# Performance work log

Measured on AMD Instinct MI355X. Metric: run time of the kernel, lower is better.

Reference implementation:

```python
import jax, jax.numpy as jnp
import numpy as np

N_NODES = 50000
N_EDGES = 800000
N_FEAT = 128
N_HID = 256
N_PAIRS = 100000


def _gcn_norm(edge_index, n_nodes):
    # add self loops, compute D^-1/2 (A+I) D^-1/2 edge weights (PyG gcn_norm)
    loops = jnp.arange(n_nodes, dtype=edge_index.dtype)
    row = jnp.concatenate([edge_index[0], loops])
    col = jnp.concatenate([edge_index[1], loops])
    deg = jax.ops.segment_sum(jnp.ones_like(col, dtype=jnp.float32), col,
                              num_segments=n_nodes)
    dinv = jnp.where(deg > 0, jax.lax.rsqrt(deg), 0.0)
    norm = dinv[row] * dinv[col]  # [E + N]
    return row, col, norm


def _gcn_conv(x, W, b, row, col, norm, n_nodes):
    h = x @ W                       # [N, out]
    msg = h[row] * norm[:, None]    # gather + scale  [E+N, out]
    agg = jax.ops.segment_sum(msg, col, num_segments=n_nodes)  # scatter-add
    return agg + b


def setup_inputs() -> dict:
    key = jax.random.key(0)
    ks = jax.random.split(key, 9)
    edge_index = jax.random.randint(ks[0], (2, N_EDGES), 0, N_NODES, dtype=jnp.int64)
    features = jax.random.normal(ks[1], (N_NODES, N_FEAT), dtype=jnp.float32)
    mask = jax.random.randint(ks[2], (N_PAIRS, 2), 0, N_NODES, dtype=jnp.int64)
    s1 = 1.0 / np.sqrt(N_FEAT)
    s2 = 1.0 / np.sqrt(N_HID)
    W1 = jax.random.uniform(ks[3], (N_FEAT, N_HID), jnp.float32, -s1, s1)
    b1 = jnp.zeros((N_HID,), jnp.float32)
    W2 = jax.random.uniform(ks[4], (N_HID, N_FEAT), jnp.float32, -s2, s2)
    b2 = jnp.zeros((N_FEAT,), jnp.float32)
    Wl = jax.random.uniform(ks[5], (N_HID, 1), jnp.float32, -s2, s2)
    bl = jax.random.uniform(ks[6], (1,), jnp.float32, -s2, s2)
    return {"edge_index": edge_index, "features": features, "mask": mask,
            "W1": W1, "b1": b1, "W2": W2, "b2": b2, "Wl": Wl, "bl": bl}


def reference(edge_index, features, mask, W1, b1, W2, b2, Wl, bl):
    n = features.shape[0]
    row, col, norm = _gcn_norm(edge_index, n)
    h = _gcn_conv(features, W1, b1, row, col, norm, n)   # GCNConv a
    h = jax.nn.relu(h)                                   # dropout p=0 -> identity
    h = _gcn_conv(h, W2, b2, row, col, norm, n)          # GCNConv b
    mt = mask.T
    p1 = jax.lax.stop_gradient(h[mt[0]])                 # .detach()
    p2 = jax.lax.stop_gradient(h[mt[1]])
    hp = jnp.concatenate([p1, p2], axis=1)               # [n_pairs, 2*n_feat]
    return jax.nn.sigmoid(hp @ Wl + bl)
```

## Files before the change

kernel.cpp:

```cpp
#include <hip/hip_runtime.h>
#include <math.h>

#define NFEAT 128
#define NHID 256
#define NBLK 128

typedef __attribute__((ext_vector_type(8))) short short8;
typedef __attribute__((ext_vector_type(4))) float f32x4;

__device__ inline unsigned short f2bf(float f) {
  unsigned u = __float_as_uint(f);
  u += 0x7fffu + ((u >> 16) & 1u);
  return (unsigned short)(u >> 16);
}
__device__ inline float bflo(unsigned u) { return __uint_as_float(u << 16); }
__device__ inline float bfhi(unsigned u) { return __uint_as_float(u & 0xffff0000u); }


__global__ __launch_bounds__(1024) void k_hist2(const int* __restrict__ col,
                                                int* __restrict__ hist2d,
                                                int nE, int nb) {
  __shared__ int h[1024];
  for (int i = threadIdx.x; i < nb; i += 1024) h[i] = 0;
  __syncthreads();
  int chunk = (nE + NBLK - 1) / NBLK;
  int beg = blockIdx.x * chunk, end = min(beg + chunk, nE);
  for (int e = beg + threadIdx.x; e < end; e += 1024)
    atomicAdd(&h[col[e] >> 6], 1);
  __syncthreads();
  for (int i = threadIdx.x; i < nb; i += 1024)
    hist2d[i * NBLK + blockIdx.x] = h[i];
}

__global__ __launch_bounds__(256) void k_bsum(const int* __restrict__ a,
                                              int* __restrict__ psum, int S) {
  int i = blockIdx.x * 256 + threadIdx.x;
  int v = (i < S) ? a[i] : 0;
#pragma unroll
  for (int o = 32; o; o >>= 1) v += __shfl_down(v, o);
  __shared__ int ws[4];
  if ((threadIdx.x & 63) == 0) ws[threadIdx.x >> 6] = v;
  __syncthreads();
  if (threadIdx.x == 0) psum[blockIdx.x] = ws[0] + ws[1] + ws[2] + ws[3];
}

__global__ __launch_bounds__(1024) void k_s2(const int* __restrict__ psum,
                                             int* __restrict__ pbase, int nc) {
  __shared__ int sh[1024];
  int t = threadIdx.x;
  int v = (t < nc) ? psum[t] : 0;
  sh[t] = v;
  __syncthreads();
  for (int o = 1; o < 1024; o <<= 1) {
    int u = (t >= o) ? sh[t - o] : 0;
    __syncthreads();
    sh[t] += u;
    __syncthreads();
  }
  if (t < nc) pbase[t] = sh[t] - v;
}

__global__ __launch_bounds__(256) void k_s3(const int* __restrict__ a,
                                            const int* __restrict__ pbase,
                                            int* __restrict__ out, int S) {
  __shared__ int sh[256];
  int t = threadIdx.x;
  int i = blockIdx.x * 256 + t;
  int d = (i < S) ? a[i] : 0;
  sh[t] = d;
  __syncthreads();
  for (int o = 1; o < 256; o <<= 1) {
    int u = (t >= o) ? sh[t - o] : 0;
    __syncthreads();
    sh[t] += u;
    __syncthreads();
  }
  if (i < S) out[i] = pbase[blockIdx.x] + sh[t] - d;
}

__global__ __launch_bounds__(1024) void k_part2(const int* __restrict__ row,
                                                const int* __restrict__ col,
                                                const int* __restrict__ sbase,
                                                unsigned* __restrict__ tmp,
                                                int nE, int nb) {
  __shared__ int cur[1024];
  for (int i = threadIdx.x; i < nb; i += 1024)
    cur[i] = sbase[i * NBLK + blockIdx.x];
  __syncthreads();
  int chunk = (nE + NBLK - 1) / NBLK;
  int beg = blockIdx.x * chunk, end = min(beg + chunk, nE);
  for (int e = beg + threadIdx.x; e < end; e += 1024) {
    int c = col[e];
    int pos = atomicAdd(&cur[c >> 6], 1);
    tmp[pos] = ((unsigned)(c & 63) << 16) | (unsigned)row[e];
  }
}

__global__ __launch_bounds__(256) void k_bsort(const unsigned* __restrict__ tmp,
                                               const int* __restrict__ sbase,
                                               int* __restrict__ ebuf,
                                               int* __restrict__ offs,
                                               float* __restrict__ dinv, int n,
                                               int nE, int nb) {
  __shared__ int bins[64], cur[64];
  int b = blockIdx.x;
  int beg = sbase[b * NBLK];
  int end = (b == nb - 1) ? nE : sbase[(b + 1) * NBLK];
  int t = threadIdx.x;
  if (t == 0 && b == nb - 1) offs[n] = nE;
  if (t < 64) bins[t] = 0;
  __syncthreads();
  for (int i = beg + t; i < end; i += 256) atomicAdd(&bins[tmp[i] >> 16], 1);
  __syncthreads();
  if (t < 64) {
    int v = bins[t];
    int s = v;
#pragma unroll
    for (int o = 1; o < 64; o <<= 1) {
      int u = __shfl_up(s, o);
      if (t >= o) s += u;
    }
    int off = beg + s - v;
    cur[t] = off;
    int node = b * 64 + t;
    if (node < n) {
      offs[node] = off;
      dinv[node] = rsqrtf((float)(v + 1));
    }
  }
  __syncthreads();
  for (int i = beg + t; i < end; i += 256) {
    unsigned p = tmp[i];
    int pos = atomicAdd(&cur[p >> 16], 1);
    ebuf[pos] = (int)(p & 0xffffu);
  }
}

__device__ inline void packOne(const float* __restrict__ W,
                               unsigned short* __restrict__ Wp, int idx, int KS,
                               int OUT) {
  int lane = idx & 63;
  int t = idx >> 6;
  int ks = t % KS;
  int nt = t / KS;
  int n = nt * 16 + (lane & 15);
  int k0 = ks * 32 + (lane >> 4) * 8;
  unsigned short v[8];
#pragma unroll
  for (int j = 0; j < 8; j++) v[j] = f2bf(W[(size_t)(k0 + j) * OUT + n]);
  *reinterpret_cast<short8*>(Wp + (size_t)idx * 8) =
      *reinterpret_cast<short8*>(v);
}

__global__ __launch_bounds__(256) void k_packW_both(
    const float* __restrict__ W1, const float* __restrict__ W2,
    unsigned short* __restrict__ W1p, unsigned short* __restrict__ W2p) {
  int idx = blockIdx.x * 256 + threadIdx.x;
  if (idx < 4096) packOne(W1, W1p, idx, 4, 256);
  else packOne(W2, W2p, idx - 4096, 8, 128);
}

__global__ __launch_bounds__(256) void k_cvt(const float* __restrict__ X,
                                             const float* __restrict__ dinv,
                                             unsigned short* __restrict__ xs,
                                             int n) {
  int i4 = blockIdx.x * 256 + threadIdx.x;
  if (i4 >= n * 32) return;
  int row = i4 >> 5;
  float4 v = reinterpret_cast<const float4*>(X)[i4];
  float d = dinv[row];
  unsigned short o[4] = {f2bf(v.x * d), f2bf(v.y * d), f2bf(v.z * d),
                         f2bf(v.w * d)};
  reinterpret_cast<ushort4*>(xs)[i4] = *reinterpret_cast<ushort4*>(o);
}

__global__ __launch_bounds__(256) void k_agg_bf(
    const unsigned int* __restrict__ G, const int* __restrict__ offs,
    const int* __restrict__ ebuf, const float* __restrict__ dinv,
    unsigned int* __restrict__ OUTP, int n) {
  int node = blockIdx.x * 4 + (threadIdx.x >> 6);
  if (node >= n) return;
  int lane = threadIdx.x & 63;
  int beg = offs[node], end = offs[node + 1];
  unsigned su = G[(size_t)node * 64 + lane];
  float a0 = bflo(su), a1 = bfhi(su);
  int e = beg;
  for (; e + 4 <= end; e += 4) {
    int s0 = ebuf[e], s1 = ebuf[e + 1], s2 = ebuf[e + 2], s3 = ebuf[e + 3];
    unsigned v0 = G[(size_t)s0 * 64 + lane];
    unsigned v1 = G[(size_t)s1 * 64 + lane];
    unsigned v2 = G[(size_t)s2 * 64 + lane];
    unsigned v3 = G[(size_t)s3 * 64 + lane];
    a0 += bflo(v0) + bflo(v1) + bflo(v2) + bflo(v3);
    a1 += bfhi(v0) + bfhi(v1) + bfhi(v2) + bfhi(v3);
  }
  for (; e < end; e++) {
    unsigned v = G[(size_t)ebuf[e] * 64 + lane];
    a0 += bflo(v);
    a1 += bfhi(v);
  }
  float d = dinv[node];
  OUTP[(size_t)node * 64 + lane] =
      (unsigned)f2bf(a0 * d) | ((unsigned)f2bf(a1 * d) << 16);
}

__global__ __launch_bounds__(256) void k_agg_q(
    const unsigned int* __restrict__ G, const int* __restrict__ offs,
    const int* __restrict__ ebuf, const float* __restrict__ dinv,
    const float* __restrict__ b2, const float* __restrict__ Wl,
    float2* __restrict__ q, int n) {
  int node = blockIdx.x * 4 + (threadIdx.x >> 6);
  if (node >= n) return;
  int lane = threadIdx.x & 63;
  int beg = offs[node], end = offs[node + 1];
  unsigned su = G[(size_t)node * 64 + lane];
  float a0 = bflo(su), a1 = bfhi(su);
  int e = beg;
  for (; e + 4 <= end; e += 4) {
    int s0 = ebuf[e], s1 = ebuf[e + 1], s2 = ebuf[e + 2], s3 = ebuf[e + 3];
    unsigned v0 = G[(size_t)s0 * 64 + lane];
    unsigned v1 = G[(size_t)s1 * 64 + lane];
    unsigned v2 = G[(size_t)s2 * 64 + lane];
    unsigned v3 = G[(size_t)s3 * 64 + lane];
    a0 += bflo(v0) + bflo(v1) + bflo(v2) + bflo(v3);
    a1 += bfhi(v0) + bfhi(v1) + bfhi(v2) + bfhi(v3);
  }
  for (; e < end; e++) {
    unsigned v = G[(size_t)ebuf[e] * 64 + lane];
    a0 += bflo(v);
    a1 += bfhi(v);
  }
  float d = dinv[node];
  a0 = a0 * d + b2[2 * lane];
  a1 = a1 * d + b2[2 * lane + 1];
  float q1 = a0 * Wl[2 * lane] + a1 * Wl[2 * lane + 1];
  float q2 = a0 * Wl[128 + 2 * lane] + a1 * Wl[129 + 2 * lane];
#pragma unroll
  for (int o = 32; o; o >>= 1) {
    q1 += __shfl_down(q1, o);
    q2 += __shfl_down(q2, o);
  }
  if (lane == 0) q[node] = make_float2(q1, q2);
}

__global__ __launch_bounds__(256) void k_mfma_fused(
    const unsigned short* __restrict__ A, const unsigned short* __restrict__ B1p,
    const unsigned short* __restrict__ B2p, const float* __restrict__ b1,
    const float* __restrict__ dinv, unsigned short* __restrict__ G2) {
  __shared__ unsigned short sh1[32 * 264];
  int rt0 = blockIdx.x * 2;
  int wave = threadIdx.x >> 6;
  int lane = threadIdx.x & 63;
  int quad = lane >> 4;
  int mrow0 = rt0 * 16 + (lane & 15);

  f32x4 acc[2][4] = {};
  const short8* Ap0 =
      reinterpret_cast<const short8*>(A + (size_t)mrow0 * NFEAT + quad * 8);
  const short8* Ap1 = reinterpret_cast<const short8*>(
      A + (size_t)(mrow0 + 16) * NFEAT + quad * 8);
#pragma unroll
  for (int ks = 0; ks < 4; ks++) {
    short8 a0 = Ap0[ks * 4];
    short8 a1 = Ap1[ks * 4];
#pragma unroll
    for (int ct = 0; ct < 4; ct++) {
      int nt = wave * 4 + ct;
      short8 b = *reinterpret_cast<const short8*>(
          B1p + ((size_t)(nt * 4 + ks) * 64 + lane) * 8);
      acc[0][ct] = __builtin_amdgcn_mfma_f32_16x16x32_bf16(a0, b, acc[0][ct], 0, 0, 0);
      acc[1][ct] = __builtin_amdgcn_mfma_f32_16x16x32_bf16(a1, b, acc[1][ct], 0, 0, 0);
    }
  }
#pragma unroll
  for (int ct = 0; ct < 4; ct++) {
    int c = (wave * 4 + ct) * 16 + (lane & 15);
    float bv = b1[c];
#pragma unroll
    for (int rg = 0; rg < 2; rg++)
#pragma unroll
      for (int i = 0; i < 4; i++) {
        float v = fmaxf(acc[rg][ct][i] + bv, 0.f);
        sh1[(rg * 16 + quad * 4 + i) * 264 + c] = f2bf(v);
      }
  }
  __syncthreads();

  f32x4 acc2[2][2] = {};
  const unsigned short* a2_0 = sh1 + (size_t)(lane & 15) * 264 + quad * 8;
  const unsigned short* a2_1 = sh1 + (size_t)(16 + (lane & 15)) * 264 + quad * 8;
#pragma unroll
  for (int ks = 0; ks < 8; ks++) {
    short8 a0 = *reinterpret_cast<const short8*>(a2_0 + ks * 32);
    short8 a1 = *reinterpret_cast<const short8*>(a2_1 + ks * 32);
#pragma unroll
    for (int ct = 0; ct < 2; ct++) {
      int nt = wave * 2 + ct;
      short8 b = *reinterpret_cast<const short8*>(
          B2p + ((size_t)(nt * 8 + ks) * 64 + lane) * 8);
      acc2[0][ct] = __builtin_amdgcn_mfma_f32_16x16x32_bf16(a0, b, acc2[0][ct], 0, 0, 0);
      acc2[1][ct] = __builtin_amdgcn_mfma_f32_16x16x32_bf16(a1, b, acc2[1][ct], 0, 0, 0);
    }
  }
#pragma unroll
  for (int rg = 0; rg < 2; rg++) {
    int r0 = (rt0 + rg) * 16 + quad * 4;
    float dv[4];
#pragma unroll
    for (int i = 0; i < 4; i++) dv[i] = dinv[r0 + i];
#pragma unroll
    for (int ct = 0; ct < 2; ct++) {
      int c = (wave * 2 + ct) * 16 + (lane & 15);
#pragma unroll
      for (int i = 0; i < 4; i++)
        G2[(size_t)(r0 + i) * NFEAT + c] = f2bf(acc2[rg][ct][i] * dv[i]);
    }
  }
}

__global__ __launch_bounds__(256) void k_head2(const float2* __restrict__ q,
                                               const int* __restrict__ mask,
                                               const float* __restrict__ bl,
                                               float* __restrict__ out, int P) {
  int p = blockIdx.x * 256 + threadIdx.x;
  if (p >= P) return;
  int m0 = mask[2 * p], m1 = mask[2 * p + 1];
  float s = q[m0].x + q[m1].y + bl[0];
  out[p] = 1.0f / (1.0f + expf(-s));
}

extern "C" void kernel_launch(void* const* d_in, const int* in_sizes, int n_in,
                              void* d_out, int out_size, void* d_ws,
                              size_t ws_size, hipStream_t stream) {
  const int* edge = (const int*)d_in[0];
  const float* feat = (const float*)d_in[1];
  const int* mask = (const int*)d_in[2];
  const float* W1 = (const float*)d_in[3];
  const float* b1 = (const float*)d_in[4];
  const float* W2 = (const float*)d_in[5];
  const float* b2 = (const float*)d_in[6];
  const float* Wl = (const float*)d_in[7];
  const float* bl = (const float*)d_in[8];
  float* out = (float*)d_out;

  const int E = in_sizes[0] / 2;
  const int N = in_sizes[1] / NFEAT;
  const int P = in_sizes[2] / 2;
  const int* rowp = edge;
  const int* colp = edge + E;
  const int nrt = N / 16;
  const int nb = (N + 63) / 64;
  const int S = nb * NBLK;
  const int nS = (S + 255) / 256;

  auto aln = [](size_t x) { return (x + 255) & ~(size_t)255; };
  const size_t rowSlack = (size_t)16 * NFEAT * 2;
  char* w = (char*)d_ws;
  int* hist2d = (int*)w;           w += aln((size_t)S * 4);
  int* sbase = (int*)w;            w += aln((size_t)S * 4);
  int* psum = (int*)w;             w += aln((size_t)1024 * 4);
  int* pbase = (int*)w;            w += aln((size_t)1024 * 4);
  int* offs = (int*)w;             w += aln((size_t)(N + 1) * 4);
  int* ebuf = (int*)w;             w += aln((size_t)E * 4);
  unsigned* tmp = (unsigned*)w;    w += aln((size_t)E * 4);
  float* dinv = (float*)w;         w += aln((size_t)N * 4 + 1024);
  unsigned short* xs = (unsigned short*)w;  w += aln((size_t)N * NFEAT * 2);
  unsigned short* z = (unsigned short*)w;   w += aln((size_t)N * NFEAT * 2 + rowSlack);
  unsigned short* g2 = (unsigned short*)w;  w += aln((size_t)N * NFEAT * 2 + rowSlack);
  float2* q = (float2*)w;          w += aln((size_t)N * 8);
  unsigned short* W1p = (unsigned short*)w; w += aln((size_t)NFEAT * NHID * 2);
  unsigned short* W2p = (unsigned short*)w; w += aln((size_t)NHID * NFEAT * 2);

  k_hist2<<<NBLK, 1024, 0, stream>>>(colp, hist2d, E, nb);
  k_bsum<<<nS, 256, 0, stream>>>(hist2d, psum, S);
  k_s2<<<1, 1024, 0, stream>>>(psum, pbase, nS);
  k_s3<<<nS, 256, 0, stream>>>(hist2d, pbase, sbase, S);
  k_part2<<<NBLK, 1024, 0, stream>>>(rowp, colp, sbase, tmp, E, nb);
  k_bsort<<<nb, 256, 0, stream>>>(tmp, sbase, ebuf, offs, dinv, N, E, nb);
  k_packW_both<<<32, 256, 0, stream>>>(W1, W2, W1p, W2p);

  k_cvt<<<(N * 32 + 255) / 256, 256, 0, stream>>>(feat, dinv, xs, N);
  k_agg_bf<<<(N + 3) / 4, 256, 0, stream>>>((const unsigned*)xs, offs, ebuf,
                                            dinv, (unsigned*)z, N);
  k_mfma_fused<<<(nrt + 1) / 2, 256, 0, stream>>>(z, W1p, W2p, b1, dinv, g2);
  k_agg_q<<<(N + 3) / 4, 256, 0, stream>>>((const unsigned*)g2, offs, ebuf,
                                           dinv, b2, Wl, q, N);
  k_head2<<<(P + 255) / 256, 256, 0, stream>>>(q, mask, bl, out, P);
}
```

Baseline: 216.9 us.

## Fuse weight packing, feature conversion, and first aggregation into neighboring kernels

Weight packing is folded into the histogram kernel as extra blocks, and the feature scale-and-convert is folded into the bucket-sort kernel using per-block dinv held in shared memory. The first-layer neighbor aggregation now runs inside the MFMA kernel, which writes the aggregated rows to shared memory instead of a global z buffer. This removes three launches and a full N×128 bf16 round trip through global memory. In exchange, the fused layer kernel handles 32 nodes per block with only 4 waves, so there is less parallelism to hide gather latency than in the old 4-nodes-per-block aggregation.

```diff
diff --git a/kernel.cpp b/kernel.cpp
--- a/kernel.cpp
+++ b/kernel.cpp
@@ -16,125 +16,6 @@
 __device__ inline float bflo(unsigned u) { return __uint_as_float(u << 16); }
 __device__ inline float bfhi(unsigned u) { return __uint_as_float(u & 0xffff0000u); }
 
-
-__global__ __launch_bounds__(1024) void k_hist2(const int* __restrict__ col,
-                                                int* __restrict__ hist2d,
-                                                int nE, int nb) {
-  __shared__ int h[1024];
-  for (int i = threadIdx.x; i < nb; i += 1024) h[i] = 0;
-  __syncthreads();
-  int chunk = (nE + NBLK - 1) / NBLK;
-  int beg = blockIdx.x * chunk, end = min(beg + chunk, nE);
-  for (int e = beg + threadIdx.x; e < end; e += 1024)
-    atomicAdd(&h[col[e] >> 6], 1);
-  __syncthreads();
-  for (int i = threadIdx.x; i < nb; i += 1024)
-    hist2d[i * NBLK + blockIdx.x] = h[i];
-}
-
-__global__ __launch_bounds__(256) void k_bsum(const int* __restrict__ a,
-                                              int* __restrict__ psum, int S) {
-  int i = blockIdx.x * 256 + threadIdx.x;
-  int v = (i < S) ? a[i] : 0;
-#pragma unroll
-  for (int o = 32; o; o >>= 1) v += __shfl_down(v, o);
-  __shared__ int ws[4];
-  if ((threadIdx.x & 63) == 0) ws[threadIdx.x >> 6] = v;
-  __syncthreads();
-  if (threadIdx.x == 0) psum[blockIdx.x] = ws[0] + ws[1] + ws[2] + ws[3];
-}
-
-__global__ __launch_bounds__(1024) void k_s2(const int* __restrict__ psum,
-                                             int* __restrict__ pbase, int nc) {
-  __shared__ int sh[1024];
-  int t = threadIdx.x;
-  int v = (t < nc) ? psum[t] : 0;
-  sh[t] = v;
-  __syncthreads();
-  for (int o = 1; o < 1024; o <<= 1) {
-    int u = (t >= o) ? sh[t - o] : 0;
-    __syncthreads();
-    sh[t] += u;
-    __syncthreads();
-  }
-  if (t < nc) pbase[t] = sh[t] - v;
-}
-
-__global__ __launch_bounds__(256) void k_s3(const int* __restrict__ a,
-                                            const int* __restrict__ pbase,
-                                            int* __restrict__ out, int S) {
-  __shared__ int sh[256];
-  int t = threadIdx.x;
-  int i = blockIdx.x * 256 + t;
-  int d = (i < S) ? a[i] : 0;
-  sh[t] = d;
-  __syncthreads();
-  for (int o = 1; o < 256; o <<= 1) {
-    int u = (t >= o) ? sh[t - o] : 0;
-    __syncthreads();
-    sh[t] += u;
-    __syncthreads();
-  }
-  if (i < S) out[i] = pbase[blockIdx.x] + sh[t] - d;
-}
-
-__global__ __launch_bounds__(1024) void k_part2(const int* __restrict__ row,
-                                                const int* __restrict__ col,
-                                                const int* __restrict__ sbase,
-                                                unsigned* __restrict__ tmp,
-                                                int nE, int nb) {
-  __shared__ int cur[1024];
-  for (int i = threadIdx.x; i < nb; i += 1024)
-    cur[i] = sbase[i * NBLK + blockIdx.x];
-  __syncthreads();
-  int chunk = (nE + NBLK - 1) / NBLK;
-  int beg = blockIdx.x * chunk, end = min(beg + chunk, nE);
-  for (int e = beg + threadIdx.x; e < end; e += 1024) {
-    int c = col[e];
-    int pos = atomicAdd(&cur[c >> 6], 1);
-    tmp[pos] = ((unsigned)(c & 63) << 16) | (unsigned)row[e];
-  }
-}
-
-__global__ __launch_bounds__(256) void k_bsort(const unsigned* __restrict__ tmp,
-                                               const int* __restrict__ sbase,
-                                               int* __restrict__ ebuf,
-                                               int* __restrict__ offs,
-                                               float* __restrict__ dinv, int n,
-                                               int nE, int nb) {
-  __shared__ int bins[64], cur[64];
-  int b = blockIdx.x;
-  int beg = sbase[b * NBLK];
-  int end = (b == nb - 1) ? nE : sbase[(b + 1) * NBLK];
-  int t = threadIdx.x;
-  if (t == 0 && b == nb - 1) offs[n] = nE;
-  if (t < 64) bins[t] = 0;
-  __syncthreads();
-  for (int i = beg + t; i < end; i += 256) atomicAdd(&bins[tmp[i] >> 16], 1);
-  __syncthreads();
-  if (t < 64) {
-    int v = bins[t];
-    int s = v;
-#pragma unroll
-    for (int o = 1; o < 64; o <<= 1) {
-      int u = __shfl_up(s, o);
-      if (t >= o) s += u;
-    }
-    int off = beg + s - v;
-    cur[t] = off;
-    int node = b * 64 + t;
-    if (node < n) {
-      offs[node] = off;
-      dinv[node] = rsqrtf((float)(v + 1));
-    }
-  }
-  __syncthreads();
-  for (int i = beg + t; i < end; i += 256) {
-    unsigned p = tmp[i];
-    int pos = atomicAdd(&cur[p >> 16], 1);
-    ebuf[pos] = (int)(p & 0xffffu);
-  }
-}
 
 __device__ inline void packOne(const float* __restrict__ W,
                                unsigned short* __restrict__ Wp, int idx, int KS,
@@ -152,56 +33,246 @@
       *reinterpret_cast<short8*>(v);
 }
 
-__global__ __launch_bounds__(256) void k_packW_both(
+__global__ __launch_bounds__(1024) void k_hist_pack(
+    const int* __restrict__ col, int* __restrict__ hist2d, int nE, int nb,
     const float* __restrict__ W1, const float* __restrict__ W2,
     unsigned short* __restrict__ W1p, unsigned short* __restrict__ W2p) {
-  int idx = blockIdx.x * 256 + threadIdx.x;
-  if (idx < 4096) packOne(W1, W1p, idx, 4, 256);
-  else packOne(W2, W2p, idx - 4096, 8, 128);
-}
-
-__global__ __launch_bounds__(256) void k_cvt(const float* __restrict__ X,
-                                             const float* __restrict__ dinv,
-                                             unsigned short* __restrict__ xs,
-                                             int n) {
-  int i4 = blockIdx.x * 256 + threadIdx.x;
-  if (i4 >= n * 32) return;
-  int row = i4 >> 5;
-  float4 v = reinterpret_cast<const float4*>(X)[i4];
-  float d = dinv[row];
-  unsigned short o[4] = {f2bf(v.x * d), f2bf(v.y * d), f2bf(v.z * d),
-                         f2bf(v.w * d)};
-  reinterpret_cast<ushort4*>(xs)[i4] = *reinterpret_cast<ushort4*>(o);
-}
-
-__global__ __launch_bounds__(256) void k_agg_bf(
-    const unsigned int* __restrict__ G, const int* __restrict__ offs,
+  if (blockIdx.x >= NBLK) {
+    int idx = (blockIdx.x - NBLK) * 1024 + threadIdx.x;
+    if (idx < 4096) packOne(W1, W1p, idx, 4, 256);
+    else packOne(W2, W2p, idx - 4096, 8, 128);
+    return;
+  }
+  __shared__ int h[1024];
+  for (int i = threadIdx.x; i < nb; i += 1024) h[i] = 0;
+  __syncthreads();
+  int chunk = (nE + NBLK - 1) / NBLK;
+  int beg = blockIdx.x * chunk, end = min(beg + chunk, nE);
+  for (int e = beg + threadIdx.x; e < end; e += 1024)
+    atomicAdd(&h[col[e] >> 6], 1);
+  __syncthreads();
+  for (int i = threadIdx.x; i < nb; i += 1024)
+    hist2d[i * NBLK + blockIdx.x] = h[i];
+}
+
+__global__ __launch_bounds__(256) void k_bsum(const int* __restrict__ a,
+                                              int* __restrict__ psum, int S) {
+  int i = blockIdx.x * 256 + threadIdx.x;
+  int v = (i < S) ? a[i] : 0;
+#pragma unroll
+  for (int o = 32; o; o >>= 1) v += __shfl_down(v, o);
+  __shared__ int ws[4];
+  if ((threadIdx.x & 63) == 0) ws[threadIdx.x >> 6] = v;
+  __syncthreads();
+  if (threadIdx.x == 0) psum[blockIdx.x] = ws[0] + ws[1] + ws[2] + ws[3];
+}
+
+__global__ __launch_bounds__(1024) void k_s2(const int* __restrict__ psum,
+                                             int* __restrict__ pbase, int nc) {
+  __shared__ int sh[1024];
+  int t = threadIdx.x;
+  int v = (t < nc) ? psum[t] : 0;
+  sh[t] = v;
+  __syncthreads();
+  for (int o = 1; o < 1024; o <<= 1) {
+    int u = (t >= o) ? sh[t - o] : 0;
+    __syncthreads();
+    sh[t] += u;
+    __syncthreads();
+  }
+  if (t < nc) pbase[t] = sh[t] - v;
+}
+
+__global__ __launch_bounds__(256) void k_s3(const int* __restrict__ a,
+                                            const int* __restrict__ pbase,
+                                            int* __restrict__ out, int S) {
+  __shared__ int sh[256];
+  int t = threadIdx.x;
+  int i = blockIdx.x * 256 + t;
+  int d = (i < S) ? a[i] : 0;
+  sh[t] = d;
+  __syncthreads();
+  for (int o = 1; o < 256; o <<= 1) {
+    int u = (t >= o) ? sh[t - o] : 0;
+    __syncthreads();
+    sh[t] += u;
+    __syncthreads();
+  }
+  if (i < S) out[i] = pbase[blockIdx.x] + sh[t] - d;
+}
+
+__global__ __launch_bounds__(1024) void k_part2(const int* __restrict__ row,
+                                                const int* __restrict__ col,
+                                                const int* __restrict__ sbase,
+                                                unsigned* __restrict__ tmp,
+                                                int nE, int nb) {
+  __shared__ int cur[1024];
+  for (int i = threadIdx.x; i < nb; i += 1024)
+    cur[i] = sbase[i * NBLK + blockIdx.x];
+  __syncthreads();
+  int chunk = (nE + NBLK - 1) / NBLK;
+  int beg = blockIdx.x * chunk, end = min(beg + chunk, nE);
+  for (int e = beg + threadIdx.x; e < end; e += 1024) {
+    int c = col[e];
+    int pos = atomicAdd(&cur[c >> 6], 1);
+    tmp[pos] = ((unsigned)(c & 63) << 16) | (unsigned)row[e];
+  }
+}
+
+__global__ __launch_bounds__(256) void k_bsort_cvt(
+    const unsigned* __restrict__ tmp, const int* __restrict__ sbase,
+    int* __restrict__ ebuf, int* __restrict__ offs, float* __restrict__ dinv,
+    const float* __restrict__ feat, unsigned short* __restrict__ xs, int n,
+    int nE, int nb) {
+  __shared__ int bins[64], cur[64];
+  __shared__ float sdinv[64];
+  int b = blockIdx.x;
+  int beg = sbase[b * NBLK];
+  int end = (b == nb - 1) ? nE : sbase[(b + 1) * NBLK];
+  int t = threadIdx.x;
+  if (t == 0 && b == nb - 1) offs[n] = nE;
+  if (t < 64) bins[t] = 0;
+  __syncthreads();
+  for (int i = beg + t; i < end; i += 256) atomicAdd(&bins[tmp[i] >> 16], 1);
+  __syncthreads();
+  if (t < 64) {
+    int v = bins[t];
+    int s = v;
+#pragma unroll
+    for (int o = 1; o < 64; o <<= 1) {
+      int u = __shfl_up(s, o);
+      if (t >= o) s += u;
+    }
+    int off = beg + s - v;
+    cur[t] = off;
+    float dv = rsqrtf((float)(v + 1));
+    sdinv[t] = dv;
+    int node = b * 64 + t;
+    if (node < n) {
+      offs[node] = off;
+      dinv[node] = dv;
+    }
+  }
+  __syncthreads();
+  for (int i = beg + t; i < end; i += 256) {
+    unsigned p = tmp[i];
+    int pos = atomicAdd(&cur[p >> 16], 1);
+    ebuf[pos] = (int)(p & 0xffffu);
+  }
+  for (int i = t; i < 64 * 32; i += 256) {
+    int r = i >> 5;
+    int node = b * 64 + r;
+    if (node >= n) break;
+    float d = sdinv[r];
+    float4 v = reinterpret_cast<const float4*>(feat)[(size_t)node * 32 + (i & 31)];
+    unsigned short o[4] = {f2bf(v.x * d), f2bf(v.y * d), f2bf(v.z * d),
+                           f2bf(v.w * d)};
+    reinterpret_cast<ushort4*>(xs)[(size_t)node * 32 + (i & 31)] =
+        *reinterpret_cast<ushort4*>(o);
+  }
+}
+
+__global__ __launch_bounds__(256) void k_fused_layer(
+    const unsigned* __restrict__ xs, const int* __restrict__ offs,
     const int* __restrict__ ebuf, const float* __restrict__ dinv,
-    unsigned int* __restrict__ OUTP, int n) {
-  int node = blockIdx.x * 4 + (threadIdx.x >> 6);
-  if (node >= n) return;
+    const unsigned short* __restrict__ B1p, const unsigned short* __restrict__ B2p,
+    const float* __restrict__ b1, unsigned short* __restrict__ G2, int n) {
+  __shared__ unsigned short zt[32 * 136];
+  __shared__ unsigned short sh1[32 * 264];
+  int wave = threadIdx.x >> 6;
   int lane = threadIdx.x & 63;
-  int beg = offs[node], end = offs[node + 1];
-  unsigned su = G[(size_t)node * 64 + lane];
-  float a0 = bflo(su), a1 = bfhi(su);
-  int e = beg;
-  for (; e + 4 <= end; e += 4) {
-    int s0 = ebuf[e], s1 = ebuf[e + 1], s2 = ebuf[e + 2], s3 = ebuf[e + 3];
-    unsigned v0 = G[(size_t)s0 * 64 + lane];
-    unsigned v1 = G[(size_t)s1 * 64 + lane];
-    unsigned v2 = G[(size_t)s2 * 64 + lane];
-    unsigned v3 = G[(size_t)s3 * 64 + lane];
-    a0 += bflo(v0) + bflo(v1) + bflo(v2) + bflo(v3);
-    a1 += bfhi(v0) + bfhi(v1) + bfhi(v2) + bfhi(v3);
-  }
-  for (; e < end; e++) {
-    unsigned v = G[(size_t)ebuf[e] * 64 + lane];
-    a0 += bflo(v);
-    a1 += bfhi(v);
-  }
-  float d = dinv[node];
-  OUTP[(size_t)node * 64 + lane] =
-      (unsigned)f2bf(a0 * d) | ((unsigned)f2bf(a1 * d) << 16);
+  int r0 = blockIdx.x * 32;
+
+  for (int j = 0; j < 8; j++) {
+    int node = r0 + wave * 8 + j;
+    unsigned outw = 0;
+    if (node < n) {
+      int beg = offs[node], end = offs[node + 1];
+      unsigned su = xs[(size_t)node * 64 + lane];
+      float a0 = bflo(su), a1 = bfhi(su);
+      int e = beg;
+      for (; e + 4 <= end; e += 4) {
+        int s0 = ebuf[e], s1 = ebuf[e + 1], s2 = ebuf[e + 2], s3 = ebuf[e + 3];
+        unsigned v0 = xs[(size_t)s0 * 64 + lane];
+        unsigned v1 = xs[(size_t)s1 * 64 + lane];
+        unsigned v2 = xs[(size_t)s2 * 64 + lane];
+        unsigned v3 = xs[(size_t)s3 * 64 + lane];
+        a0 += bflo(v0) + bflo(v1) + bflo(v2) + bflo(v3);
+        a1 += bfhi(v0) + bfhi(v1) + bfhi(v2) + bfhi(v3);
+      }
+      for (; e < end; e++) {
+        unsigned v = xs[(size_t)ebuf[e] * 64 + lane];
+        a0 += bflo(v);
+        a1 += bfhi(v);
+      }
+      float d = dinv[node];
+      outw = (unsigned)f2bf(a0 * d) | ((unsigned)f2bf(a1 * d) << 16);
+    }
+    *reinterpret_cast<unsigned*>(&zt[(wave * 8 + j) * 136 + lane * 2]) = outw;
+  }
+  __syncthreads();
+
+  int quad = lane >> 4;
+  f32x4 acc[2][4] = {};
+  const unsigned short* za0 = zt + (size_t)(lane & 15) * 136 + quad * 8;
+  const unsigned short* za1 = zt + (size_t)(16 + (lane & 15)) * 136 + quad * 8;
+#pragma unroll
+  for (int ks = 0; ks < 4; ks++) {
+    short8 a0 = *reinterpret_cast<const short8*>(za0 + ks * 32);
+    short8 a1 = *reinterpret_cast<const short8*>(za1 + ks * 32);
+#pragma unroll
+    for (int ct = 0; ct < 4; ct++) {
+      int nt = wave * 4 + ct;
+      short8 b = *reinterpret_cast<const short8*>(
+          B1p + ((size_t)(nt * 4 + ks) * 64 + lane) * 8);
+      acc[0][ct] = __builtin_amdgcn_mfma_f32_16x16x32_bf16(a0, b, acc[0][ct], 0, 0, 0);
+      acc[1][ct] = __builtin_amdgcn_mfma_f32_16x16x32_bf16(a1, b, acc[1][ct], 0, 0, 0);
+    }
+  }
+#pragma unroll
+  for (int ct = 0; ct < 4; ct++) {
+    int c = (wave * 4 + ct) * 16 + (lane & 15);
+    float bv = b1[c];
+#pragma unroll
+    for (int rg = 0; rg < 2; rg++)
+#pragma unroll
+      for (int i = 0; i < 4; i++) {
+        float v = fmaxf(acc[rg][ct][i] + bv, 0.f);
+        sh1[(rg * 16 + quad * 4 + i) * 264 + c] = f2bf(v);
+      }
+  }
+  __syncthreads();
+
+  f32x4 acc2[2][2] = {};
+  const unsigned short* a2_0 = sh1 + (size_t)(lane & 15) * 264 + quad * 8;
+  const unsigned short* a2_1 = sh1 + (size_t)(16 + (lane & 15)) * 264 + quad * 8;
+#pragma unroll
+  for (int ks = 0; ks < 8; ks++) {
+    short8 a0 = *reinterpret_cast<const short8*>(a2_0 + ks * 32);
+    short8 a1 = *reinterpret_cast<const short8*>(a2_1 + ks * 32);
+#pragma unroll
+    for (int ct = 0; ct < 2; ct++) {
+      int nt = wave * 2 + ct;
+      short8 b = *reinterpret_cast<const short8*>(
+          B2p + ((size_t)(nt * 8 + ks) * 64 + lane) * 8);
+      acc2[0][ct] = __builtin_amdgcn_mfma_f32_16x16x32_bf16(a0, b, acc2[0][ct], 0, 0, 0);
+      acc2[1][ct] = __builtin_amdgcn_mfma_f32_16x16x32_bf16(a1, b, acc2[1][ct], 0, 0, 0);
+    }
+  }
+#pragma unroll
+  for (int rg = 0; rg < 2; rg++) {
+    int rr = r0 + rg * 16 + quad * 4;
+    float dv[4];
+#pragma unroll
+    for (int i = 0; i < 4; i++) dv[i] = dinv[rr + i];
+#pragma unroll
+    for (int ct = 0; ct < 2; ct++) {
+      int c = (wave * 2 + ct) * 16 + (lane & 15);
+#pragma unroll
+      for (int i = 0; i < 4; i++)
+        G2[(size_t)(rr + i) * NFEAT + c] = f2bf(acc2[rg][ct][i] * dv[i]);
+    }
+  }
 }
 
 __global__ __launch_bounds__(256) void k_agg_q(
@@ -243,81 +314,6 @@
   if (lane == 0) q[node] = make_float2(q1, q2);
 }
 
-__global__ __launch_bounds__(256) void k_mfma_fused(
-    const unsigned short* __restrict__ A, const unsigned short* __restrict__ B1p,
-    const unsigned short* __restrict__ B2p, const float* __restrict__ b1,
-    const float* __restrict__ dinv, unsigned short* __restrict__ G2) {
-  __shared__ unsigned short sh1[32 * 264];
-  int rt0 = blockIdx.x * 2;
-  int wave = threadIdx.x >> 6;
-  int lane = threadIdx.x & 63;
-  int quad = lane >> 4;
-  int mrow0 = rt0 * 16 + (lane & 15);
-
-  f32x4 acc[2][4] = {};
-  const short8* Ap0 =
-      reinterpret_cast<const short8*>(A + (size_t)mrow0 * NFEAT + quad * 8);
-  const short8* Ap1 = reinterpret_cast<const short8*>(
-      A + (size_t)(mrow0 + 16) * NFEAT + quad * 8);
-#pragma unroll
-  for (int ks = 0; ks < 4; ks++) {
-    short8 a0 = Ap0[ks * 4];
-    short8 a1 = Ap1[ks * 4];
-#pragma unroll
-    for (int ct = 0; ct < 4; ct++) {
-      int nt = wave * 4 + ct;
-      short8 b = *reinterpret_cast<const short8*>(
-          B1p + ((size_t)(nt * 4 + ks) * 64 + lane) * 8);
-      acc[0][ct] = __builtin_amdgcn_mfma_f32_16x16x32_bf16(a0, b, acc[0][ct], 0, 0, 0);
-      acc[1][ct] = __builtin_amdgcn_mfma_f32_16x16x32_bf16(a1, b, acc[1][ct], 0, 0, 0);
-    }
-  }
-#pragma unroll
-  for (int ct = 0; ct < 4; ct++) {
-    int c = (wave * 4 + ct) * 16 + (lane & 15);
-    float bv = b1[c];
-#pragma unroll
-    for (int rg = 0; rg < 2; rg++)
-#pragma unroll
-      for (int i = 0; i < 4; i++) {
-        float v = fmaxf(acc[rg][ct][i] + bv, 0.f);
-        sh1[(rg * 16 + quad * 4 + i) * 264 + c] = f2bf(v);
-      }
-  }
-  __syncthreads();
-
-  f32x4 acc2[2][2] = {};
-  const unsigned short* a2_0 = sh1 + (size_t)(lane & 15) * 264 + quad * 8;
-  const unsigned short* a2_1 = sh1 + (size_t)(16 + (lane & 15)) * 264 + quad * 8;
-#pragma unroll
-  for (int ks = 0; ks < 8; ks++) {
-    short8 a0 = *reinterpret_cast<const short8*>(a2_0 + ks * 32);
-    short8 a1 = *reinterpret_cast<const short8*>(a2_1 + ks * 32);
-#pragma unroll
-    for (int ct = 0; ct < 2; ct++) {
-      int nt = wave * 2 + ct;
-      short8 b = *reinterpret_cast<const short8*>(
-          B2p + ((size_t)(nt * 8 + ks) * 64 + lane) * 8);
-      acc2[0][ct] = __builtin_amdgcn_mfma_f32_16x16x32_bf16(a0, b, acc2[0][ct], 0, 0, 0);
-      acc2[1][ct] = __builtin_amdgcn_mfma_f32_16x16x32_bf16(a1, b, acc2[1][ct], 0, 0, 0);
-    }
-  }
-#pragma unroll
-  for (int rg = 0; rg < 2; rg++) {
-    int r0 = (rt0 + rg) * 16 + quad * 4;
-    float dv[4];
-#pragma unroll
-    for (int i = 0; i < 4; i++) dv[i] = dinv[r0 + i];
-#pragma unroll
-    for (int ct = 0; ct < 2; ct++) {
-      int c = (wave * 2 + ct) * 16 + (lane & 15);
-#pragma unroll
-      for (int i = 0; i < 4; i++)
-        G2[(size_t)(r0 + i) * NFEAT + c] = f2bf(acc2[rg][ct][i] * dv[i]);
-    }
-  }
-}
-
 __global__ __launch_bounds__(256) void k_head2(const float2* __restrict__ q,
                                                const int* __restrict__ mask,
                                                const float* __restrict__ bl,
@@ -365,24 +361,21 @@
   unsigned* tmp = (unsigned*)w;    w += aln((size_t)E * 4);
   float* dinv = (float*)w;         w += aln((size_t)N * 4 + 1024);
   unsigned short* xs = (unsigned short*)w;  w += aln((size_t)N * NFEAT * 2);
-  unsigned short* z = (unsigned short*)w;   w += aln((size_t)N * NFEAT * 2 + rowSlack);
   unsigned short* g2 = (unsigned short*)w;  w += aln((size_t)N * NFEAT * 2 + rowSlack);
   float2* q = (float2*)w;          w += aln((size_t)N * 8);
   unsigned short* W1p = (unsigned short*)w; w += aln((size_t)NFEAT * NHID * 2);
   unsigned short* W2p = (unsigned short*)w; w += aln((size_t)NHID * NFEAT * 2);
 
-  k_hist2<<<NBLK, 1024, 0, stream>>>(colp, hist2d, E, nb);
+  k_hist_pack<<<NBLK + 8, 1024, 0, stream>>>(colp, hist2d, E, nb, W1, W2, W1p,
+                                             W2p);
   k_bsum<<<nS, 256, 0, stream>>>(hist2d, psum, S);
   k_s2<<<1, 1024, 0, stream>>>(psum, pbase, nS);
   k_s3<<<nS, 256, 0, stream>>>(hist2d, pbase, sbase, S);
   k_part2<<<NBLK, 1024, 0, stream>>>(rowp, colp, sbase, tmp, E, nb);
-  k_bsort<<<nb, 256, 0, stream>>>(tmp, sbase, ebuf, offs, dinv, N, E, nb);
-  k_packW_both<<<32, 256, 0, stream>>>(W1, W2, W1p, W2p);
-
-  k_cvt<<<(N * 32 + 255) / 256, 256, 0, stream>>>(feat, dinv, xs, N);
-  k_agg_bf<<<(N + 3) / 4, 256, 0, stream>>>((const unsigned*)xs, offs, ebuf,
-                                            dinv, (unsigned*)z, N);
-  k_mfma_fused<<<(nrt + 1) / 2, 256, 0, stream>>>(z, W1p, W2p, b1, dinv, g2);
+  k_bsort_cvt<<<nb, 256, 0, stream>>>(tmp, sbase, ebuf, offs, dinv, feat, xs,
+                                      N, E, nb);
+  k_fused_layer<<<(nrt + 1) / 2, 256, 0, stream>>>(
+      (const unsigned*)xs, offs, ebuf, dinv, W1p, W2p, b1, g2, N);
   k_agg_q<<<(N + 3) / 4, 256, 0, stream>>>((const unsigned*)g2, offs, ebuf,
                                            dinv, b2, Wl, q, N);
   k_head2<<<(P + 255) / 256, 256, 0, stream>>>(q, mask, bl, out, P);
```

After: 231.1 us. 6.5% more time.

## Fuse preprocessing kernels to cut launch count in the graph build

Applied to the files above, without the earlier changes.

Merges the weight packing into the histogram kernel as extra blocks, folds the single-block prefix scan into the per-block scan by having each block reduce the preceding partial sums, and fuses the feature bf16 conversion into the bucket-sort kernel using per-bucket dinv kept in shared memory. This removes three kernel launches and their serialization gaps from the preprocessing chain. In exchange, each scan block redundantly sums up to a few hundred partial sums, and the conversion now runs on only nb blocks of 256 threads, which may lower parallelism for that memory-bound step.

```diff
diff --git a/kernel.cpp b/kernel.cpp
--- a/kernel.cpp
+++ b/kernel.cpp
@@ -16,125 +16,6 @@
 __device__ inline float bflo(unsigned u) { return __uint_as_float(u << 16); }
 __device__ inline float bfhi(unsigned u) { return __uint_as_float(u & 0xffff0000u); }
 
-
-__global__ __launch_bounds__(1024) void k_hist2(const int* __restrict__ col,
-                                                int* __restrict__ hist2d,
-                                                int nE, int nb) {
-  __shared__ int h[1024];
-  for (int i = threadIdx.x; i < nb; i += 1024) h[i] = 0;
-  __syncthreads();
-  int chunk = (nE + NBLK - 1) / NBLK;
-  int beg = blockIdx.x * chunk, end = min(beg + chunk, nE);
-  for (int e = beg + threadIdx.x; e < end; e += 1024)
-    atomicAdd(&h[col[e] >> 6], 1);
-  __syncthreads();
-  for (int i = threadIdx.x; i < nb; i += 1024)
-    hist2d[i * NBLK + blockIdx.x] = h[i];
-}
-
-__global__ __launch_bounds__(256) void k_bsum(const int* __restrict__ a,
-                                              int* __restrict__ psum, int S) {
-  int i = blockIdx.x * 256 + threadIdx.x;
-  int v = (i < S) ? a[i] : 0;
-#pragma unroll
-  for (int o = 32; o; o >>= 1) v += __shfl_down(v, o);
-  __shared__ int ws[4];
-  if ((threadIdx.x & 63) == 0) ws[threadIdx.x >> 6] = v;
-  __syncthreads();
-  if (threadIdx.x == 0) psum[blockIdx.x] = ws[0] + ws[1] + ws[2] + ws[3];
-}
-
-__global__ __launch_bounds__(1024) void k_s2(const int* __restrict__ psum,
-                                             int* __restrict__ pbase, int nc) {
-  __shared__ int sh[1024];
-  int t = threadIdx.x;
-  int v = (t < nc) ? psum[t] : 0;
-  sh[t] = v;
-  __syncthreads();
-  for (int o = 1; o < 1024; o <<= 1) {
-    int u = (t >= o) ? sh[t - o] : 0;
-    __syncthreads();
-    sh[t] += u;
-    __syncthreads();
-  }
-  if (t < nc) pbase[t] = sh[t] - v;
-}
-
-__global__ __launch_bounds__(256) void k_s3(const int* __restrict__ a,
-                                            const int* __restrict__ pbase,
-                                            int* __restrict__ out, int S) {
-  __shared__ int sh[256];
-  int t = threadIdx.x;
-  int i = blockIdx.x * 256 + t;
-  int d = (i < S) ? a[i] : 0;
-  sh[t] = d;
-  __syncthreads();
-  for (int o = 1; o < 256; o <<= 1) {
-    int u = (t >= o) ? sh[t - o] : 0;
-    __syncthreads();
-    sh[t] += u;
-    __syncthreads();
-  }
-  if (i < S) out[i] = pbase[blockIdx.x] + sh[t] - d;
-}
-
-__global__ __launch_bounds__(1024) void k_part2(const int* __restrict__ row,
-                                                const int* __restrict__ col,
-                                                const int* __restrict__ sbase,
-                                                unsigned* __restrict__ tmp,
-                                                int nE, int nb) {
-  __shared__ int cur[1024];
-  for (int i = threadIdx.x; i < nb; i += 1024)
-    cur[i] = sbase[i * NBLK + blockIdx.x];
-  __syncthreads();
-  int chunk = (nE + NBLK - 1) / NBLK;
-  int beg = blockIdx.x * chunk, end = min(beg + chunk, nE);
-  for (int e = beg + threadIdx.x; e < end; e += 1024) {
-    int c = col[e];
-    int pos = atomicAdd(&cur[c >> 6], 1);
-    tmp[pos] = ((unsigned)(c & 63) << 16) | (unsigned)row[e];
-  }
-}
-
-__global__ __launch_bounds__(256) void k_bsort(const unsigned* __restrict__ tmp,
-                                               const int* __restrict__ sbase,
-                                               int* __restrict__ ebuf,
-                                               int* __restrict__ offs,
-                                               float* __restrict__ dinv, int n,
-                                               int nE, int nb) {
-  __shared__ int bins[64], cur[64];
-  int b = blockIdx.x;
-  int beg = sbase[b * NBLK];
-  int end = (b == nb - 1) ? nE : sbase[(b + 1) * NBLK];
-  int t = threadIdx.x;
-  if (t == 0 && b == nb - 1) offs[n] = nE;
-  if (t < 64) bins[t] = 0;
-  __syncthreads();
-  for (int i = beg + t; i < end; i += 256) atomicAdd(&bins[tmp[i] >> 16], 1);
-  __syncthreads();
-  if (t < 64) {
-    int v = bins[t];
-    int s = v;
-#pragma unroll
-    for (int o = 1; o < 64; o <<= 1) {
-      int u = __shfl_up(s, o);
-      if (t >= o) s += u;
-    }
-    int off = beg + s - v;
-    cur[t] = off;
-    int node = b * 64 + t;
-    if (node < n) {
-      offs[node] = off;
-      dinv[node] = rsqrtf((float)(v + 1));
-    }
-  }
-  __syncthreads();
-  for (int i = beg + t; i < end; i += 256) {
-    unsigned p = tmp[i];
-    int pos = atomicAdd(&cur[p >> 16], 1);
-    ebuf[pos] = (int)(p & 0xffffu);
-  }
-}
 
 __device__ inline void packOne(const float* __restrict__ W,
                                unsigned short* __restrict__ Wp, int idx, int KS,
@@ -152,26 +33,135 @@
       *reinterpret_cast<short8*>(v);
 }
 
-__global__ __launch_bounds__(256) void k_packW_both(
+__global__ __launch_bounds__(1024) void k_hist_pack(
+    const int* __restrict__ col, int* __restrict__ hist2d, int nE, int nb,
     const float* __restrict__ W1, const float* __restrict__ W2,
     unsigned short* __restrict__ W1p, unsigned short* __restrict__ W2p) {
-  int idx = blockIdx.x * 256 + threadIdx.x;
-  if (idx < 4096) packOne(W1, W1p, idx, 4, 256);
-  else packOne(W2, W2p, idx - 4096, 8, 128);
-}
-
-__global__ __launch_bounds__(256) void k_cvt(const float* __restrict__ X,
-                                             const float* __restrict__ dinv,
-                                             unsigned short* __restrict__ xs,
-                                             int n) {
-  int i4 = blockIdx.x * 256 + threadIdx.x;
-  if (i4 >= n * 32) return;
-  int row = i4 >> 5;
-  float4 v = reinterpret_cast<const float4*>(X)[i4];
-  float d = dinv[row];
-  unsigned short o[4] = {f2bf(v.x * d), f2bf(v.y * d), f2bf(v.z * d),
-                         f2bf(v.w * d)};
-  reinterpret_cast<ushort4*>(xs)[i4] = *reinterpret_cast<ushort4*>(o);
+  if (blockIdx.x >= NBLK) {
+    int idx = (blockIdx.x - NBLK) * 1024 + threadIdx.x;
+    if (idx < 4096) packOne(W1, W1p, idx, 4, 256);
+    else packOne(W2, W2p, idx - 4096, 8, 128);
+    return;
+  }
+  __shared__ int h[1024];
+  for (int i = threadIdx.x; i < nb; i += 1024) h[i] = 0;
+  __syncthreads();
+  int chunk = (nE + NBLK - 1) / NBLK;
+  int beg = blockIdx.x * chunk, end = min(beg + chunk, nE);
+  for (int e = beg + threadIdx.x; e < end; e += 1024)
+    atomicAdd(&h[col[e] >> 6], 1);
+  __syncthreads();
+  for (int i = threadIdx.x; i < nb; i += 1024)
+    hist2d[i * NBLK + blockIdx.x] = h[i];
+}
+
+__global__ __launch_bounds__(256) void k_bsum(const int* __restrict__ a,
+                                              int* __restrict__ psum, int S) {
+  int i = blockIdx.x * 256 + threadIdx.x;
+  int v = (i < S) ? a[i] : 0;
+#pragma unroll
+  for (int o = 32; o; o >>= 1) v += __shfl_down(v, o);
+  __shared__ int ws[4];
+  if ((threadIdx.x & 63) == 0) ws[threadIdx.x >> 6] = v;
+  __syncthreads();
+  if (threadIdx.x == 0) psum[blockIdx.x] = ws[0] + ws[1] + ws[2] + ws[3];
+}
+
+__global__ __launch_bounds__(256) void k_s3m(const int* __restrict__ a,
+                                             const int* __restrict__ psum,
+                                             int* __restrict__ out, int S) {
+  __shared__ int sh[256];
+  __shared__ int ws[4];
+  int t = threadIdx.x;
+  int b = blockIdx.x;
+  int partial = 0;
+  for (int i = t; i < b; i += 256) partial += psum[i];
+#pragma unroll
+  for (int o = 32; o; o >>= 1) partial += __shfl_down(partial, o);
+  if ((t & 63) == 0) ws[t >> 6] = partial;
+  int i = b * 256 + t;
+  int d = (i < S) ? a[i] : 0;
+  sh[t] = d;
+  __syncthreads();
+  int base = ws[0] + ws[1] + ws[2] + ws[3];
+  for (int o = 1; o < 256; o <<= 1) {
+    int u = (t >= o) ? sh[t - o] : 0;
+    __syncthreads();
+    sh[t] += u;
+    __syncthreads();
+  }
+  if (i < S) out[i] = base + sh[t] - d;
+}
+
+__global__ __launch_bounds__(1024) void k_part2(const int* __restrict__ row,
+                                                const int* __restrict__ col,
+                                                const int* __restrict__ sbase,
+                                                unsigned* __restrict__ tmp,
+                                                int nE, int nb) {
+  __shared__ int cur[1024];
+  for (int i = threadIdx.x; i < nb; i += 1024)
+    cur[i] = sbase[i * NBLK + blockIdx.x];
+  __syncthreads();
+  int chunk = (nE + NBLK - 1) / NBLK;
+  int beg = blockIdx.x * chunk, end = min(beg + chunk, nE);
+  for (int e = beg + threadIdx.x; e < end; e += 1024) {
+    int c = col[e];
+    int pos = atomicAdd(&cur[c >> 6], 1);
+    tmp[pos] = ((unsigned)(c & 63) << 16) | (unsigned)row[e];
+  }
+}
+
+__global__ __launch_bounds__(256) void k_bsort_cvt(
+    const unsigned* __restrict__ tmp, const int* __restrict__ sbase,
+    int* __restrict__ ebuf, int* __restrict__ offs, float* __restrict__ dinv,
+    const float* __restrict__ feat, unsigned short* __restrict__ xs, int n,
+    int nE, int nb) {
+  __shared__ int bins[64], cur[64];
+  __shared__ float sdinv[64];
+  int b = blockIdx.x;
+  int beg = sbase[b * NBLK];
+  int end = (b == nb - 1) ? nE : sbase[(b + 1) * NBLK];
+  int t = threadIdx.x;
+  if (t == 0 && b == nb - 1) offs[n] = nE;
+  if (t < 64) bins[t] = 0;
+  __syncthreads();
+  for (int i = beg + t; i < end; i += 256) atomicAdd(&bins[tmp[i] >> 16], 1);
+  __syncthreads();
+  if (t < 64) {
+    int v = bins[t];
+    int s = v;
+#pragma unroll
+    for (int o = 1; o < 64; o <<= 1) {
+      int u = __shfl_up(s, o);
+      if (t >= o) s += u;
+    }
+    int off = beg + s - v;
+    cur[t] = off;
+    float dv = rsqrtf((float)(v + 1));
+    sdinv[t] = dv;
+    int node = b * 64 + t;
+    if (node < n) {
+      offs[node] = off;
+      dinv[node] = dv;
+    }
+  }
+  __syncthreads();
+  for (int i = beg + t; i < end; i += 256) {
+    unsigned p = tmp[i];
+    int pos = atomicAdd(&cur[p >> 16], 1);
+    ebuf[pos] = (int)(p & 0xffffu);
+  }
+  for (int i = t; i < 64 * 32; i += 256) {
+    int r = i >> 5;
+    int node = b * 64 + r;
+    if (node >= n) break;
+    float d = sdinv[r];
+    float4 v = reinterpret_cast<const float4*>(feat)[(size_t)node * 32 + (i & 31)];
+    unsigned short o[4] = {f2bf(v.x * d), f2bf(v.y * d), f2bf(v.z * d),
+                           f2bf(v.w * d)};
+    reinterpret_cast<ushort4*>(xs)[(size_t)node * 32 + (i & 31)] =
+        *reinterpret_cast<ushort4*>(o);
+  }
 }
 
 __global__ __launch_bounds__(256) void k_agg_bf(
@@ -202,6 +192,81 @@
   float d = dinv[node];
   OUTP[(size_t)node * 64 + lane] =
       (unsigned)f2bf(a0 * d) | ((unsigned)f2bf(a1 * d) << 16);
+}
+
+__global__ __launch_bounds__(256) void k_mfma_fused(
+    const unsigned short* __restrict__ A, const unsigned short* __restrict__ B1p,
+    const unsigned short* __restrict__ B2p, const float* __restrict__ b1,
+    const float* __restrict__ dinv, unsigned short* __restrict__ G2) {
+  __shared__ unsigned short sh1[32 * 264];
+  int rt0 = blockIdx.x * 2;
+  int wave = threadIdx.x >> 6;
+  int lane = threadIdx.x & 63;
+  int quad = lane >> 4;
+  int mrow0 = rt0 * 16 + (lane & 15);
+
+  f32x4 acc[2][4] = {};
+  const short8* Ap0 =
+      reinterpret_cast<const short8*>(A + (size_t)mrow0 * NFEAT + quad * 8);
+  const short8* Ap1 = reinterpret_cast<const short8*>(
+      A + (size_t)(mrow0 + 16) * NFEAT + quad * 8);
+#pragma unroll
+  for (int ks = 0; ks < 4; ks++) {
+    short8 a0 = Ap0[ks * 4];
+    short8 a1 = Ap1[ks * 4];
+#pragma unroll
+    for (int ct = 0; ct < 4; ct++) {
+      int nt = wave * 4 + ct;
+      short8 b = *reinterpret_cast<const short8*>(
+          B1p + ((size_t)(nt * 4 + ks) * 64 + lane) * 8);
+      acc[0][ct] = __builtin_amdgcn_mfma_f32_16x16x32_bf16(a0, b, acc[0][ct], 0, 0, 0);
+      acc[1][ct] = __builtin_amdgcn_mfma_f32_16x16x32_bf16(a1, b, acc[1][ct], 0, 0, 0);
+    }
+  }
+#pragma unroll
+  for (int ct = 0; ct < 4; ct++) {
+    int c = (wave * 4 + ct) * 16 + (lane & 15);
+    float bv = b1[c];
+#pragma unroll
+    for (int rg = 0; rg < 2; rg++)
+#pragma unroll
+      for (int i = 0; i < 4; i++) {
+        float v = fmaxf(acc[rg][ct][i] + bv, 0.f);
+        sh1[(rg * 16 + quad * 4 + i) * 264 + c] = f2bf(v);
+      }
+  }
+  __syncthreads();
+
+  f32x4 acc2[2][2] = {};
+  const unsigned short* a2_0 = sh1 + (size_t)(lane & 15) * 264 + quad * 8;
+  const unsigned short* a2_1 = sh1 + (size_t)(16 + (lane & 15)) * 264 + quad * 8;
+#pragma unroll
+  for (int ks = 0; ks < 8; ks++) {
+    short8 a0 = *reinterpret_cast<const short8*>(a2_0 + ks * 32);
+    short8 a1 = *reinterpret_cast<const short8*>(a2_1 + ks * 32);
+#pragma unroll
+    for (int ct = 0; ct < 2; ct++) {
+      int nt = wave * 2 + ct;
+      short8 b = *reinterpret_cast<const short8*>(
+          B2p + ((size_t)(nt * 8 + ks) * 64 + lane) * 8);
+      acc2[0][ct] = __builtin_amdgcn_mfma_f32_16x16x32_bf16(a0, b, acc2[0][ct], 0, 0, 0);
+      acc2[1][ct] = __builtin_amdgcn_mfma_f32_16x16x32_bf16(a1, b, acc2[1][ct], 0, 0, 0);
+    }
+  }
+#pragma unroll
+  for (int rg = 0; rg < 2; rg++) {
+    int r0 = (rt0 + rg) * 16 + quad * 4;
+    float dv[4];
+#pragma unroll
+    for (int i = 0; i < 4; i++) dv[i] = dinv[r0 + i];
+#pragma unroll
+    for (int ct = 0; ct < 2; ct++) {
+      int c = (wave * 2 + ct) * 16 + (lane & 15);
+#pragma unroll
+      for (int i = 0; i < 4; i++)
+        G2[(size_t)(r0 + i) * NFEAT + c] = f2bf(acc2[rg][ct][i] * dv[i]);
+    }
+  }
 }
 
 __global__ __launch_bounds__(256) void k_agg_q(
@@ -243,81 +308,6 @@
   if (lane == 0) q[node] = make_float2(q1, q2);
 }
 
-__global__ __launch_bounds__(256) void k_mfma_fused(
-    const unsigned short* __restrict__ A, const unsigned short* __restrict__ B1p,
-    const unsigned short* __restrict__ B2p, const float* __restrict__ b1,
-    const float* __restrict__ dinv, unsigned short* __restrict__ G2) {
-  __shared__ unsigned short sh1[32 * 264];
-  int rt0 = blockIdx.x * 2;
-  int wave = threadIdx.x >> 6;
-  int lane = threadIdx.x & 63;
-  int quad = lane >> 4;
-  int mrow0 = rt0 * 16 + (lane & 15);
-
-  f32x4 acc[2][4] = {};
-  const short8* Ap0 =
-      reinterpret_cast<const short8*>(A + (size_t)mrow0 * NFEAT + quad * 8);
-  const short8* Ap1 = reinterpret_cast<const short8*>(
-      A + (size_t)(mrow0 + 16) * NFEAT + quad * 8);
-#pragma unroll
-  for (int ks = 0; ks < 4; ks++) {
-    short8 a0 = Ap0[ks * 4];
-    short8 a1 = Ap1[ks * 4];
-#pragma unroll
-    for (int ct = 0; ct < 4; ct++) {
-      int nt = wave * 4 + ct;
-      short8 b = *reinterpret_cast<const short8*>(
-          B1p + ((size_t)(nt * 4 + ks) * 64 + lane) * 8);
-      acc[0][ct] = __builtin_amdgcn_mfma_f32_16x16x32_bf16(a0, b, acc[0][ct], 0, 0, 0);
-      acc[1][ct] = __builtin_amdgcn_mfma_f32_16x16x32_bf16(a1, b, acc[1][ct], 0, 0, 0);
-    }
-  }
-#pragma unroll
-  for (int ct = 0; ct < 4; ct++) {
-    int c = (wave * 4 + ct) * 16 + (lane & 15);
-    float bv = b1[c];
-#pragma unroll
-    for (int rg = 0; rg < 2; rg++)
-#pragma unroll
-      for (int i = 0; i < 4; i++) {
-        float v = fmaxf(acc[rg][ct][i] + bv, 0.f);
-        sh1[(rg * 16 + quad * 4 + i) * 264 + c] = f2bf(v);
-      }
-  }
-  __syncthreads();
-
-  f32x4 acc2[2][2] = {};
-  const unsigned short* a2_0 = sh1 + (size_t)(lane & 15) * 264 + quad * 8;
-  const unsigned short* a2_1 = sh1 + (size_t)(16 + (lane & 15)) * 264 + quad * 8;
-#pragma unroll
-  for (int ks = 0; ks < 8; ks++) {
-    short8 a0 = *reinterpret_cast<const short8*>(a2_0 + ks * 32);
-    short8 a1 = *reinterpret_cast<const short8*>(a2_1 + ks * 32);
-#pragma unroll
-    for (int ct = 0; ct < 2; ct++) {
-      int nt = wave * 2 + ct;
-      short8 b = *reinterpret_cast<const short8*>(
-          B2p + ((size_t)(nt * 8 + ks) * 64 + lane) * 8);
-      acc2[0][ct] = __builtin_amdgcn_mfma_f32_16x16x32_bf16(a0, b, acc2[0][ct], 0, 0, 0);
-      acc2[1][ct] = __builtin_amdgcn_mfma_f32_16x16x32_bf16(a1, b, acc2[1][ct], 0, 0, 0);
-    }
-  }
-#pragma unroll
-  for (int rg = 0; rg < 2; rg++) {
-    int r0 = (rt0 + rg) * 16 + quad * 4;
-    float dv[4];
-#pragma unroll
-    for (int i = 0; i < 4; i++) dv[i] = dinv[r0 + i];
-#pragma unroll
-    for (int ct = 0; ct < 2; ct++) {
-      int c = (wave * 2 + ct) * 16 + (lane & 15);
-#pragma unroll
-      for (int i = 0; i < 4; i++)
-        G2[(size_t)(r0 + i) * NFEAT + c] = f2bf(acc2[rg][ct][i] * dv[i]);
-    }
-  }
-}
-
 __global__ __launch_bounds__(256) void k_head2(const float2* __restrict__ q,
                                                const int* __restrict__ mask,
                                                const float* __restrict__ bl,
@@ -359,7 +349,6 @@
   int* hist2d = (int*)w;           w += aln((size_t)S * 4);
   int* sbase = (int*)w;            w += aln((size_t)S * 4);
   int* psum = (int*)w;             w += aln((size_t)1024 * 4);
-  int* pbase = (int*)w;            w += aln((size_t)1024 * 4);
   int* offs = (int*)w;             w += aln((size_t)(N + 1) * 4);
   int* ebuf = (int*)w;             w += aln((size_t)E * 4);
   unsigned* tmp = (unsigned*)w;    w += aln((size_t)E * 4);
@@ -371,15 +360,13 @@
   unsigned short* W1p = (unsigned short*)w; w += aln((size_t)NFEAT * NHID * 2);
   unsigned short* W2p = (unsigned short*)w; w += aln((size_t)NHID * NFEAT * 2);
 
-  k_hist2<<<NBLK, 1024, 0, stream>>>(colp, hist2d, E, nb);
+  k_hist_pack<<<NBLK + 8, 1024, 0, stream>>>(colp, hist2d, E, nb, W1, W2, W1p,
+                                             W2p);
   k_bsum<<<nS, 256, 0, stream>>>(hist2d, psum, S);
-  k_s2<<<1, 1024, 0, stream>>>(psum, pbase, nS);
-  k_s3<<<nS, 256, 0, stream>>>(hist2d, pbase, sbase, S);
+  k_s3m<<<nS, 256, 0, stream>>>(hist2d, psum, sbase, S);
   k_part2<<<NBLK, 1024, 0, stream>>>(rowp, colp, sbase, tmp, E, nb);
-  k_bsort<<<nb, 256, 0, stream>>>(tmp, sbase, ebuf, offs, dinv, N, E, nb);
-  k_packW_both<<<32, 256, 0, stream>>>(W1, W2, W1p, W2p);
-
-  k_cvt<<<(N * 32 + 255) / 256, 256, 0, stream>>>(feat, dinv, xs, N);
+  k_bsort_cvt<<<nb, 256, 0, stream>>>(tmp, sbase, ebuf, offs, dinv, feat, xs,
+                                      N, E, nb);
   k_agg_bf<<<(N + 3) / 4, 256, 0, stream>>>((const unsigned*)xs, offs, ebuf,
                                             dinv, (unsigned*)z, N);
   k_mfma_fused<<<(nrt + 1) / 2, 256, 0, stream>>>(z, W1p, W2p, b1, dinv, g2);
```

After: 215.9 us. About the same (-0.5%).
